# Kernel optimization log

Hardware: AMD Instinct MI355X
Metric: run time of the kernel (lower is better)

## Reference

```python
import jax, jax.numpy as jnp
import numpy as np

DIM = 512
HEADS = 8        # MultiHeadAttention default heads=8 (init 'heads' arg actually sets dim_head)
DIM_HEAD = 64    # from AttentionLayers heads=64 passed positionally as dim_head
HIDDEN = HEADS * DIM_HEAD  # 512
EPS = 1e-5


def setup_inputs() -> dict:
    key = jax.random.key(0)
    ks = jax.random.split(key, 8)
    s = 1.0 / np.sqrt(DIM)
    return {
        "x": jax.random.normal(ks[0], (4, 2048, DIM), dtype=jnp.float32),
        "ln_g": jnp.ones((DIM,), dtype=jnp.float32),
        "ln_b": jnp.zeros((DIM,), dtype=jnp.float32),
        "Wq": jax.random.normal(ks[1], (DIM, HIDDEN), dtype=jnp.float32) * s,
        "Wk": jax.random.normal(ks[2], (DIM, HIDDEN), dtype=jnp.float32) * s,
        "Wv": jax.random.normal(ks[3], (DIM, HIDDEN), dtype=jnp.float32) * s,
        "Wo": jax.random.normal(ks[4], (HIDDEN, DIM), dtype=jnp.float32) * s,
        "bo": jnp.zeros((DIM,), dtype=jnp.float32),
    }


def reference(x, ln_g, ln_b, Wq, Wk, Wv, Wo, bo):
    b, n, d = x.shape
    residual = x
    # pre-norm LayerNorm
    mu = jnp.mean(x, axis=-1, keepdims=True)
    var = jnp.mean((x - mu) ** 2, axis=-1, keepdims=True)
    xn = (x - mu) * jax.lax.rsqrt(var + EPS) * ln_g + ln_b
    # QKV projections (no bias), split into heads: [b, s, h, dh]
    q = (xn @ Wq).reshape(b, n, HEADS, DIM_HEAD)
    k = (xn @ Wk).reshape(b, n, HEADS, DIM_HEAD)
    v = (xn @ Wv).reshape(b, n, HEADS, DIM_HEAD)
    scale = HIDDEN ** (-0.5)  # note: scales by hidden_dim, not dim_head (faithful)
    scores = jnp.einsum('bihd,bjhd->bhij', q, k) * scale  # [b,h,i,j] full matrix
    attn = jax.nn.softmax(scores, axis=-1)
    out = jnp.einsum('bhij,bjhd->bihd', attn, v).reshape(b, n, HIDDEN)
    out = out @ Wo + bo
    # residual; the subsequent FFN layer's output is discarded in the source
    return out + residual
```

## Files before the change

kernel.cpp:

```cpp
#include <hip/hip_runtime.h>
#include <hip/hip_bf16.h>

#define DIM 512
#define SEQ 2048
#define BATCH 4
#define NHEADS 8
#define DH 64
#define NROWS (BATCH * SEQ)
#define LN_EPS 1e-5f

typedef __hip_bfloat16 bf16;
typedef __attribute__((ext_vector_type(8))) short short8;
typedef __attribute__((ext_vector_type(4))) float f32x4;

#define MFMA16(a, b, c) __builtin_amdgcn_mfma_f32_16x16x32_bf16((a), (b), (c), 0, 0, 0)

#if __has_builtin(__builtin_amdgcn_exp2f)
#define EXP2(x) __builtin_amdgcn_exp2f(x)
#else
#define EXP2(x) exp2f(x)
#endif

#if defined(__has_builtin)
#if __has_builtin(__builtin_amdgcn_global_load_lds)
#define HAS_GLDS 1
#endif
#endif

__device__ __forceinline__ void glds16(const bf16* g, bf16* l) {
#ifdef HAS_GLDS
  __builtin_amdgcn_global_load_lds((const __attribute__((address_space(1))) void*)g,
                                   (__attribute__((address_space(3))) void*)l, 16, 0, 0);
#else
  *reinterpret_cast<uint4*>(l) = *reinterpret_cast<const uint4*>(g);
#endif
}

__device__ __forceinline__ void store_bf16x4(bf16* p, float a, float b, float c, float d) {
  bf16 tmp[4] = {__float2bfloat16(a), __float2bfloat16(b), __float2bfloat16(c),
                 __float2bfloat16(d)};
  *reinterpret_cast<ushort4*>(p) = *reinterpret_cast<const ushort4*>(tmp);
}

#define Q_SCALE_LOG2E 0.06375872f

__global__ void ln_kernel(const float* __restrict__ x, const float* __restrict__ gamma,
                          const float* __restrict__ beta, bf16* __restrict__ xn) {
  const int row = blockIdx.x;
  const int t = threadIdx.x;
  const float2 v = reinterpret_cast<const float2*>(x + (size_t)row * DIM)[t];
  float s = v.x + v.y;
  float ss = v.x * v.x + v.y * v.y;
#pragma unroll
  for (int off = 32; off > 0; off >>= 1) {
    s += __shfl_down(s, off);
    ss += __shfl_down(ss, off);
  }
  __shared__ float red[8];
  __shared__ float stats[2];
  if ((t & 63) == 0) { red[(t >> 6) * 2] = s; red[(t >> 6) * 2 + 1] = ss; }
  __syncthreads();
  if (t == 0) {
    float S = red[0] + red[2] + red[4] + red[6];
    float SS = red[1] + red[3] + red[5] + red[7];
    float mu = S * (1.0f / DIM);
    float var = SS * (1.0f / DIM) - mu * mu;
    stats[0] = mu;
    stats[1] = rsqrtf(var + LN_EPS);
  }
  __syncthreads();
  const float mu = stats[0], rs = stats[1];
  const float2 gg = reinterpret_cast<const float2*>(gamma)[t];
  const float2 bb = reinterpret_cast<const float2*>(beta)[t];
  __hip_bfloat162 o;
  o.x = __float2bfloat16((v.x - mu) * rs * gg.x + bb.x);
  o.y = __float2bfloat16((v.y - mu) * rs * gg.y + bb.y);
  reinterpret_cast<__hip_bfloat162*>(xn + (size_t)row * DIM)[t] = o;
}

__global__ void wt_all_kernel(const float* __restrict__ Wq, const float* __restrict__ Wk,
                              const float* __restrict__ Wv, const float* __restrict__ Wo,
                              bf16* __restrict__ Wt) {
  const int z = blockIdx.z;
  const float* __restrict__ W = (z == 0) ? Wq : (z == 1) ? Wk : (z == 2) ? Wv : Wo;
  const float scale = (z == 0) ? Q_SCALE_LOG2E : 1.0f;
  bf16* __restrict__ dst = Wt + (size_t)z * DIM * DIM;
  __shared__ float tile[32][33];
  const int bx = blockIdx.x, by = blockIdx.y;
  const int tx = threadIdx.x & 31, ty = threadIdx.x >> 5;
#pragma unroll
  for (int i = 0; i < 32; i += 8)
    tile[ty + i][tx] = W[(size_t)(by * 32 + ty + i) * DIM + bx * 32 + tx];
  __syncthreads();
#pragma unroll
  for (int i = 0; i < 32; i += 8)
    dst[(size_t)(bx * 32 + ty + i) * DIM + by * 32 + tx] =
        __float2bfloat16(tile[tx][ty + i] * scale);
}

__launch_bounds__(256, 3)
__global__ void gemm_qkv_kernel(const bf16* __restrict__ A, const bf16* __restrict__ Bt,
                                bf16* __restrict__ qo, bf16* __restrict__ ko,
                                bf16* __restrict__ vo) {
  const int m0 = blockIdx.x * 128, n0g = blockIdx.y * 128;
  __shared__ __align__(16) bf16 sA[2][128 * 32];
  __shared__ __align__(16) bf16 sB[2][128 * 32];
  const int t = threadIdx.x, w = t >> 6, l = t & 63;
  const int r = l & 15, g = l >> 4;
  const int wm = w >> 1, wn = w & 1;
  const int crow = w * 32 + (l >> 2);
  const int ccol = (l & 3) * 8;
  const bf16* gA = A + (size_t)(m0 + crow) * DIM + ccol;
  const bf16* gB = Bt + (size_t)(n0g + crow) * DIM + ccol;
  const int loff = w * 1024 + l * 8;
  f32x4 acc[4][4] = {};
  glds16(gA, sA[0] + loff);
  glds16(gA + 16 * DIM, sA[0] + loff + 512);
  glds16(gB, sB[0] + loff);
  glds16(gB + 16 * DIM, sB[0] + loff + 512);
  const int NK = DIM / 32;
  for (int ks = 0; ks < NK; ks++) {
    const int cur = ks & 1;
    __syncthreads();
    if (ks + 1 < NK) {
      const int k0n = (ks + 1) * 32;
      glds16(gA + k0n, sA[1 - cur] + loff);
      glds16(gA + 16 * DIM + k0n, sA[1 - cur] + loff + 512);
      glds16(gB + k0n, sB[1 - cur] + loff);
      glds16(gB + 16 * DIM + k0n, sB[1 - cur] + loff + 512);
    }
    short8 af[4], bfv[4];
#pragma unroll
    for (int i = 0; i < 4; i++)
      af[i] = *reinterpret_cast<const short8*>(&sA[cur][(wm * 64 + i * 16 + r) * 32 + g * 8]);
#pragma unroll
    for (int j = 0; j < 4; j++)
      bfv[j] = *reinterpret_cast<const short8*>(&sB[cur][(wn * 64 + j * 16 + r) * 32 + g * 8]);
#pragma unroll
    for (int i = 0; i < 4; i++)
#pragma unroll
      for (int j = 0; j < 4; j++) acc[i][j] = MFMA16(af[i], bfv[j], acc[i][j]);
  }
  const int z = n0g >> 9;
  const int nc0 = (n0g & 511) + wn * 64;
  bf16* __restrict__ outp = (z == 0) ? qo : (z == 1) ? ko : vo;
#pragma unroll
  for (int i = 0; i < 4; i++)
#pragma unroll
    for (int j = 0; j < 4; j++)
#pragma unroll
      for (int reg = 0; reg < 4; reg++) {
        const int m = m0 + wm * 64 + i * 16 + g * 4 + reg;
        const int col = nc0 + j * 16 + r;
        outp[(size_t)m * DIM + col] = __float2bfloat16(acc[i][j][reg]);
      }
}

__global__ void vtrans_kernel(const bf16* __restrict__ v, bf16* __restrict__ vt) {
  __shared__ __align__(16) bf16 sT[64][72];
  const int s0 = blockIdx.x * 64, d0 = blockIdx.y * 64, b = blockIdx.z;
  const int t = threadIdx.x;
  const int row = t >> 2, col = (t & 3) * 8;
  const bf16* src = v + ((size_t)(b * SEQ) + s0 + row) * DIM + d0 + col;
  reinterpret_cast<uint4&>(sT[row][col]) = *reinterpret_cast<const uint4*>(src);
  reinterpret_cast<uint4&>(sT[row][col + 32]) = *reinterpret_cast<const uint4*>(src + 32);
  __syncthreads();
  const int drow = t >> 2, jcol = (t & 3) * 8;
  bf16 tmp[8], tmp2[8];
#pragma unroll
  for (int jj = 0; jj < 8; jj++) tmp[jj] = sT[jcol + jj][drow];
#pragma unroll
  for (int jj = 0; jj < 8; jj++) tmp2[jj] = sT[jcol + 32 + jj][drow];
  bf16* dst = vt + ((size_t)(b * DIM) + d0 + drow) * SEQ + s0 + jcol;
  *reinterpret_cast<uint4*>(dst) = *reinterpret_cast<const uint4*>(tmp);
  *reinterpret_cast<uint4*>(dst + 32) = *reinterpret_cast<const uint4*>(tmp2);
}

template <bool SPLIT>
__launch_bounds__(128, 3)
__global__ void attn_kernel(const bf16* __restrict__ q, const bf16* __restrict__ k,
                            const bf16* __restrict__ vt, bf16* __restrict__ ao,
                            bf16* __restrict__ opart, float* __restrict__ lpart) {
  const int it = blockIdx.x, bh = blockIdx.y, jh = blockIdx.z;
  const int b = bh >> 3, h = bh & 7;
  const int t = threadIdx.x, wv = t >> 6, l = t & 63;
  const int r = l & 15, g = l >> 4;
  __shared__ __align__(16) bf16 sK[64 * 64];
  __shared__ __align__(16) bf16 sV[64 * 64];
  __shared__ __align__(16) bf16 sPt[2][2][16][72];
  const int i0 = it * 64 + wv * 32;
  const bf16* qp = q + ((size_t)(b * SEQ) + i0 + r) * DIM + h * DH;
  short8 qf[2][2];
#pragma unroll
  for (int s = 0; s < 2; s++)
#pragma unroll
    for (int kc = 0; kc < 2; kc++)
      qf[s][kc] = *reinterpret_cast<const short8*>(qp + s * 16 * DIM + kc * 32 + g * 8);
  f32x4 oacc[2][4] = {};
  float lsum[2] = {0.f, 0.f};
  const int jbase = SPLIT ? jh * (SEQ / 2) : 0;
  const int srow8 = l >> 3;
  const int u = ((l & 7) - srow8) & 7;
  const bf16* kg = k + ((size_t)(b * SEQ) + jbase + wv * 32 + srow8) * DIM + h * DH + u * 8;
  const bf16* vg = vt + ((size_t)(b * DIM) + h * DH + wv * 32 + srow8) * SEQ + jbase + u * 8;
  const int loff = wv * 2048 + l * 8;
  const int e0 = 64 * r + 8 * ((g + r) & 7);
  const int e1 = 64 * r + 8 * ((4 + g + r) & 7);
  const int NJ = SPLIT ? (SEQ / 2) / 64 : SEQ / 64;
  for (int jt = 0; jt < NJ; jt++) {
    const int j0 = jt * 64;
#pragma unroll
    for (int cc = 0; cc < 4; cc++) {
      glds16(kg + (size_t)(j0 + cc * 8) * DIM, sK + loff + cc * 512);
      glds16(vg + (size_t)(cc * 8) * SEQ + j0, sV + loff + cc * 512);
    }
    __syncthreads();
    f32x4 st[2][4];
#pragma unroll
    for (int c = 0; c < 4; c++) {
      const short8 kf0 = *reinterpret_cast<const short8*>(sK + 1024 * c + e0);
      const short8 kf1 = *reinterpret_cast<const short8*>(sK + 1024 * c + e1);
#pragma unroll
      for (int s = 0; s < 2; s++) {
        f32x4 a = {0.f, 0.f, 0.f, 0.f};
        a = MFMA16(kf0, qf[s][0], a);
        a = MFMA16(kf1, qf[s][1], a);
        st[s][c] = a;
      }
    }
#pragma unroll
    for (int s = 0; s < 2; s++)
#pragma unroll
      for (int c = 0; c < 4; c++) {
        const float p0 = EXP2(st[s][c][0]);
        const float p1 = EXP2(st[s][c][1]);
        const float p2 = EXP2(st[s][c][2]);
        const float p3 = EXP2(st[s][c][3]);
        lsum[s] += (p0 + p1) + (p2 + p3);
        store_bf16x4(&sPt[wv][s][r][c * 16 + g * 4], p0, p1, p2, p3);
      }
#pragma unroll
    for (int kc2 = 0; kc2 < 2; kc2++) {
      short8 pf[2];
#pragma unroll
      for (int s = 0; s < 2; s++)
        pf[s] = *reinterpret_cast<const short8*>(&sPt[wv][s][r][kc2 * 32 + g * 8]);
      const int ev = (kc2 == 0) ? e0 : e1;
#pragma unroll
      for (int dt = 0; dt < 4; dt++) {
        const short8 vf = *reinterpret_cast<const short8*>(sV + 1024 * dt + ev);
#pragma unroll
        for (int s = 0; s < 2; s++) oacc[s][dt] = MFMA16(vf, pf[s], oacc[s][dt]);
      }
    }
    __syncthreads();
  }
#pragma unroll
  for (int s = 0; s < 2; s++) {
    lsum[s] += __shfl_xor(lsum[s], 16);
    lsum[s] += __shfl_xor(lsum[s], 32);
  }
  if (SPLIT) {
    const size_t obase = ((size_t)jh * 32 + bh) * SEQ;
#pragma unroll
    for (int s = 0; s < 2; s++) {
      const int i = i0 + s * 16 + r;
      if (l < 16) lpart[obase + i] = lsum[s];
#pragma unroll
      for (int dt = 0; dt < 4; dt++)
        store_bf16x4(opart + (obase + i) * 64 + dt * 16 + g * 4, oacc[s][dt][0],
                     oacc[s][dt][1], oacc[s][dt][2], oacc[s][dt][3]);
    }
  } else {
#pragma unroll
    for (int s = 0; s < 2; s++) {
      const float inv = 1.0f / lsum[s];
      const int i = i0 + s * 16 + r;
#pragma unroll
      for (int dt = 0; dt < 4; dt++)
        store_bf16x4(ao + ((size_t)(b * SEQ) + i) * DIM + h * DH + dt * 16 + g * 4,
                     oacc[s][dt][0] * inv, oacc[s][dt][1] * inv, oacc[s][dt][2] * inv,
                     oacc[s][dt][3] * inv);
    }
  }
}

__global__ void attn_combine_kernel(const bf16* __restrict__ opart,
                                    const float* __restrict__ lpart, bf16* __restrict__ ao) {
  const int bh = blockIdx.y, b = bh >> 3, h = bh & 7;
  const int t = threadIdx.x;
  const int i = blockIdx.x * 16 + (t >> 4);
  const int d = (t & 15) * 4;
  const size_t row0 = (size_t)bh * SEQ + i;
  const size_t row1 = ((size_t)32 + bh) * SEQ + i;
  const ushort4 a = *reinterpret_cast<const ushort4*>(opart + row0 * 64 + d);
  const ushort4 c = *reinterpret_cast<const ushort4*>(opart + row1 * 64 + d);
  const float inv = 1.0f / (lpart[row0] + lpart[row1]);
#define B2F(us) __uint_as_float(((unsigned)(us)) << 16)
  store_bf16x4(ao + ((size_t)(b * SEQ) + i) * DIM + h * DH + d,
               (B2F(a.x) + B2F(c.x)) * inv, (B2F(a.y) + B2F(c.y)) * inv,
               (B2F(a.z) + B2F(c.z)) * inv, (B2F(a.w) + B2F(c.w)) * inv);
#undef B2F
}

__launch_bounds__(256, 2)
__global__ void gemm_proj_kernel(const bf16* __restrict__ A, const bf16* __restrict__ Bt,
                                 const float* __restrict__ bo, const float* __restrict__ x,
                                 float* __restrict__ out) {
  const int m0 = blockIdx.x * 128, n0 = blockIdx.y * 64;
  __shared__ __align__(16) bf16 sA[2][128 * 32];
  __shared__ __align__(16) bf16 sB[2][64 * 32];
  const int t = threadIdx.x, w = t >> 6, l = t & 63;
  const int r = l & 15, g = l >> 4;
  const int wm = w >> 1, wn = w & 1;
  const int arow = t >> 2;
  const int ccol = (t & 3) * 8;
  const bf16* gA = A + (size_t)(m0 + arow) * DIM + ccol;
  const bf16* gB = Bt + (size_t)(n0 + arow) * DIM + ccol;
  const int loff = t * 8;
  f32x4 acc[4][2] = {};
  glds16(gA, sA[0] + loff);
  glds16(gA + 64 * DIM, sA[0] + loff + 2048);
  glds16(gB, sB[0] + loff);
  const int NK = DIM / 32;
  for (int ks = 0; ks < NK; ks++) {
    const int cur = ks & 1;
    __syncthreads();
    if (ks + 1 < NK) {
      const int k0n = (ks + 1) * 32;
      glds16(gA + k0n, sA[1 - cur] + loff);
      glds16(gA + 64 * DIM + k0n, sA[1 - cur] + loff + 2048);
      glds16(gB + k0n, sB[1 - cur] + loff);
    }
    short8 af[4], bfv[2];
#pragma unroll
    for (int i = 0; i < 4; i++)
      af[i] = *reinterpret_cast<const short8*>(&sA[cur][(wm * 64 + i * 16 + r) * 32 + g * 8]);
#pragma unroll
    for (int j = 0; j < 2; j++)
      bfv[j] = *reinterpret_cast<const short8*>(&sB[cur][(wn * 32 + j * 16 + r) * 32 + g * 8]);
#pragma unroll
    for (int i = 0; i < 4; i++)
#pragma unroll
      for (int j = 0; j < 2; j++) acc[i][j] = MFMA16(af[i], bfv[j], acc[i][j]);
  }
#pragma unroll
  for (int i = 0; i < 4; i++)
#pragma unroll
    for (int j = 0; j < 2; j++)
#pragma unroll
      for (int reg = 0; reg < 4; reg++) {
        const int m = m0 + wm * 64 + i * 16 + g * 4 + reg;
        const int col = n0 + wn * 32 + j * 16 + r;
        out[(size_t)m * DIM + col] = acc[i][j][reg] + bo[col] + x[(size_t)m * DIM + col];
      }
}

extern "C" void kernel_launch(void* const* d_in, const int* in_sizes, int n_in,
                              void* d_out, int out_size, void* d_ws, size_t ws_size,
                              hipStream_t stream) {
  (void)in_sizes; (void)n_in; (void)out_size;
  const float* x    = (const float*)d_in[0];
  const float* ln_g = (const float*)d_in[1];
  const float* ln_b = (const float*)d_in[2];
  const float* Wq   = (const float*)d_in[3];
  const float* Wk   = (const float*)d_in[4];
  const float* Wv   = (const float*)d_in[5];
  const float* Wo   = (const float*)d_in[6];
  const float* bo   = (const float*)d_in[7];
  float* out = (float*)d_out;
  char* ws = (char*)d_ws;
  bf16* xn  = (bf16*)(ws);
  bf16* vtb = (bf16*)(ws);
  bf16* wt  = (bf16*)(ws + (8u << 20));
  bf16* qb  = (bf16*)(ws + (10u << 20));
  bf16* kb  = (bf16*)(ws + (18u << 20));
  bf16* vb  = (bf16*)(ws + (26u << 20));
  bf16* aob = (bf16*)(ws + (34u << 20));
  bf16* opart = (bf16*)(ws + (42u << 20));
  float* lpart = (float*)(ws + (58u << 20));
  const bool split = ws_size >= ((58u << 20) + (1u << 19));

  ln_kernel<<<NROWS, 256, 0, stream>>>(x, ln_g, ln_b, xn);
  wt_all_kernel<<<dim3(16, 16, 4), 256, 0, stream>>>(Wq, Wk, Wv, Wo, wt);
  gemm_qkv_kernel<<<dim3(NROWS / 128, (3 * DIM) / 128), 256, 0, stream>>>(xn, wt, qb, kb, vb);
  vtrans_kernel<<<dim3(SEQ / 64, DIM / 64, BATCH), 256, 0, stream>>>(vb, vtb);
  if (split) {
    attn_kernel<true><<<dim3(SEQ / 64, BATCH * NHEADS, 2), 128, 0, stream>>>(
        qb, kb, vtb, aob, opart, lpart);
    attn_combine_kernel<<<dim3(SEQ / 16, BATCH * NHEADS), 256, 0, stream>>>(opart, lpart, aob);
  } else {
    attn_kernel<false><<<dim3(SEQ / 64, BATCH * NHEADS, 1), 128, 0, stream>>>(
        qb, kb, vtb, aob, opart, lpart);
  }
  gemm_proj_kernel<<<dim3(NROWS / 128, DIM / 64), 256, 0, stream>>>(aob, wt + 3 * DIM * DIM,
                                                                    bo, x, out);
}
```

Before: 186.4 us.

## Fuse V transpose into QKV GEMM epilogue and keep K/V tiles in registers

The QKV GEMM epilogue now writes V already transposed, going through a padded LDS tile, so the separate vtrans kernel and its extra global round trip are removed. The attention kernel no longer stages K and V through shared memory with barriers. Each lane loads its own MFMA fragments straight from global memory into registers and prefetches the next tile's fragments during compute. This removes LDS traffic and per-tile __syncthreads, but each wave now loads the K/V data itself, which raises redundant global/L2 traffic and register pressure.

Result: slower. 244.3 us (+31.0%).

```diff
diff --git a/kernel.cpp b/kernel.cpp
--- a/kernel.cpp
+++ b/kernel.cpp
@@ -101,10 +101,12 @@
 __launch_bounds__(256, 3)
 __global__ void gemm_qkv_kernel(const bf16* __restrict__ A, const bf16* __restrict__ Bt,
                                 bf16* __restrict__ qo, bf16* __restrict__ ko,
-                                bf16* __restrict__ vo) {
+                                bf16* __restrict__ vto) {
   const int m0 = blockIdx.x * 128, n0g = blockIdx.y * 128;
-  __shared__ __align__(16) bf16 sA[2][128 * 32];
-  __shared__ __align__(16) bf16 sB[2][128 * 32];
+  __shared__ __align__(16) char smem[128 * 136 * 2];
+  bf16* const sA = (bf16*)smem;
+  bf16* const sB = (bf16*)(smem + 16384);
+  bf16* const sT = (bf16*)smem;
   const int t = threadIdx.x, w = t >> 6, l = t & 63;
   const int r = l & 15, g = l >> 4;
   const int wm = w >> 1, wn = w & 1;
@@ -114,66 +116,68 @@
   const bf16* gB = Bt + (size_t)(n0g + crow) * DIM + ccol;
   const int loff = w * 1024 + l * 8;
   f32x4 acc[4][4] = {};
-  glds16(gA, sA[0] + loff);
-  glds16(gA + 16 * DIM, sA[0] + loff + 512);
-  glds16(gB, sB[0] + loff);
-  glds16(gB + 16 * DIM, sB[0] + loff + 512);
+  glds16(gA, sA + loff);
+  glds16(gA + 16 * DIM, sA + loff + 512);
+  glds16(gB, sB + loff);
+  glds16(gB + 16 * DIM, sB + loff + 512);
   const int NK = DIM / 32;
   for (int ks = 0; ks < NK; ks++) {
     const int cur = ks & 1;
     __syncthreads();
     if (ks + 1 < NK) {
       const int k0n = (ks + 1) * 32;
-      glds16(gA + k0n, sA[1 - cur] + loff);
-      glds16(gA + 16 * DIM + k0n, sA[1 - cur] + loff + 512);
-      glds16(gB + k0n, sB[1 - cur] + loff);
-      glds16(gB + 16 * DIM + k0n, sB[1 - cur] + loff + 512);
+      glds16(gA + k0n, sA + (1 - cur) * 4096 + loff);
+      glds16(gA + 16 * DIM + k0n, sA + (1 - cur) * 4096 + loff + 512);
+      glds16(gB + k0n, sB + (1 - cur) * 4096 + loff);
+      glds16(gB + 16 * DIM + k0n, sB + (1 - cur) * 4096 + loff + 512);
     }
     short8 af[4], bfv[4];
 #pragma unroll
     for (int i = 0; i < 4; i++)
-      af[i] = *reinterpret_cast<const short8*>(&sA[cur][(wm * 64 + i * 16 + r) * 32 + g * 8]);
+      af[i] = *reinterpret_cast<const short8*>(
+          &sA[cur * 4096 + (wm * 64 + i * 16 + r) * 32 + g * 8]);
 #pragma unroll
     for (int j = 0; j < 4; j++)
-      bfv[j] = *reinterpret_cast<const short8*>(&sB[cur][(wn * 64 + j * 16 + r) * 32 + g * 8]);
+      bfv[j] = *reinterpret_cast<const short8*>(
+          &sB[cur * 4096 + (wn * 64 + j * 16 + r) * 32 + g * 8]);
 #pragma unroll
     for (int i = 0; i < 4; i++)
 #pragma unroll
       for (int j = 0; j < 4; j++) acc[i][j] = MFMA16(af[i], bfv[j], acc[i][j]);
   }
   const int z = n0g >> 9;
-  const int nc0 = (n0g & 511) + wn * 64;
-  bf16* __restrict__ outp = (z == 0) ? qo : (z == 1) ? ko : vo;
-#pragma unroll
-  for (int i = 0; i < 4; i++)
-#pragma unroll
-    for (int j = 0; j < 4; j++)
-#pragma unroll
-      for (int reg = 0; reg < 4; reg++) {
-        const int m = m0 + wm * 64 + i * 16 + g * 4 + reg;
-        const int col = nc0 + j * 16 + r;
-        outp[(size_t)m * DIM + col] = __float2bfloat16(acc[i][j][reg]);
-      }
-}
-
-__global__ void vtrans_kernel(const bf16* __restrict__ v, bf16* __restrict__ vt) {
-  __shared__ __align__(16) bf16 sT[64][72];
-  const int s0 = blockIdx.x * 64, d0 = blockIdx.y * 64, b = blockIdx.z;
-  const int t = threadIdx.x;
-  const int row = t >> 2, col = (t & 3) * 8;
-  const bf16* src = v + ((size_t)(b * SEQ) + s0 + row) * DIM + d0 + col;
-  reinterpret_cast<uint4&>(sT[row][col]) = *reinterpret_cast<const uint4*>(src);
-  reinterpret_cast<uint4&>(sT[row][col + 32]) = *reinterpret_cast<const uint4*>(src + 32);
-  __syncthreads();
-  const int drow = t >> 2, jcol = (t & 3) * 8;
-  bf16 tmp[8], tmp2[8];
-#pragma unroll
-  for (int jj = 0; jj < 8; jj++) tmp[jj] = sT[jcol + jj][drow];
-#pragma unroll
-  for (int jj = 0; jj < 8; jj++) tmp2[jj] = sT[jcol + 32 + jj][drow];
-  bf16* dst = vt + ((size_t)(b * DIM) + d0 + drow) * SEQ + s0 + jcol;
-  *reinterpret_cast<uint4*>(dst) = *reinterpret_cast<const uint4*>(tmp);
-  *reinterpret_cast<uint4*>(dst + 32) = *reinterpret_cast<const uint4*>(tmp2);
+  const int b = m0 / SEQ;
+  if (z != 2) {
+    bf16* __restrict__ outp = (z == 0) ? qo : ko;
+    const int nc0 = (n0g & 511) + wn * 64;
+#pragma unroll
+    for (int i = 0; i < 4; i++)
+#pragma unroll
+      for (int j = 0; j < 4; j++)
+#pragma unroll
+        for (int reg = 0; reg < 4; reg++) {
+          const int m = m0 + wm * 64 + i * 16 + g * 4 + reg;
+          const int col = nc0 + j * 16 + r;
+          outp[(size_t)m * DIM + col] = __float2bfloat16(acc[i][j][reg]);
+        }
+  } else {
+    __syncthreads();
+#pragma unroll
+    for (int i = 0; i < 4; i++)
+#pragma unroll
+      for (int j = 0; j < 4; j++)
+        store_bf16x4(&sT[(wn * 64 + j * 16 + r) * 136 + wm * 64 + i * 16 + g * 4],
+                     acc[i][j][0], acc[i][j][1], acc[i][j][2], acc[i][j][3]);
+    __syncthreads();
+    const int dr = t >> 1;
+    const int mc = (t & 1) * 64;
+    const int dcol = (n0g & 511) + dr;
+    bf16* dst = vto + ((size_t)b * DIM + dcol) * SEQ + (m0 - b * SEQ) + mc;
+#pragma unroll
+    for (int uu = 0; uu < 8; uu++)
+      *reinterpret_cast<uint4*>(dst + uu * 8) =
+          *reinterpret_cast<const uint4*>(&sT[dr * 136 + mc + uu * 8]);
+  }
 }
 
 template <bool SPLIT>
@@ -185,9 +189,7 @@
   const int b = bh >> 3, h = bh & 7;
   const int t = threadIdx.x, wv = t >> 6, l = t & 63;
   const int r = l & 15, g = l >> 4;
-  __shared__ __align__(16) bf16 sK[64 * 64];
-  __shared__ __align__(16) bf16 sV[64 * 64];
-  __shared__ __align__(16) bf16 sPt[2][2][16][72];
+  __shared__ __align__(16) bf16 sPt[2][2][16][76];
   const int i0 = it * 64 + wv * 32;
   const bf16* qp = q + ((size_t)(b * SEQ) + i0 + r) * DIM + h * DH;
   short8 qf[2][2];
@@ -199,27 +201,27 @@
   f32x4 oacc[2][4] = {};
   float lsum[2] = {0.f, 0.f};
   const int jbase = SPLIT ? jh * (SEQ / 2) : 0;
-  const int srow8 = l >> 3;
-  const int u = ((l & 7) - srow8) & 7;
-  const bf16* kg = k + ((size_t)(b * SEQ) + jbase + wv * 32 + srow8) * DIM + h * DH + u * 8;
-  const bf16* vg = vt + ((size_t)(b * DIM) + h * DH + wv * 32 + srow8) * SEQ + jbase + u * 8;
-  const int loff = wv * 2048 + l * 8;
-  const int e0 = 64 * r + 8 * ((g + r) & 7);
-  const int e1 = 64 * r + 8 * ((4 + g + r) & 7);
+  const bf16* kl = k + ((size_t)(b * SEQ) + jbase + r) * DIM + h * DH + g * 8;
+  const bf16* vl = vt + ((size_t)(b * DIM) + h * DH + r) * SEQ + jbase + g * 8;
+  uint4 kr[8], vr[8];
+#pragma unroll
+  for (int c = 0; c < 4; c++)
+#pragma unroll
+    for (int hf = 0; hf < 2; hf++)
+      kr[c * 2 + hf] = *reinterpret_cast<const uint4*>(kl + (size_t)(c * 16) * DIM + hf * 32);
+#pragma unroll
+  for (int dt = 0; dt < 4; dt++)
+#pragma unroll
+    for (int kc2 = 0; kc2 < 2; kc2++)
+      vr[dt * 2 + kc2] =
+          *reinterpret_cast<const uint4*>(vl + (size_t)(dt * 16) * SEQ + kc2 * 32);
   const int NJ = SPLIT ? (SEQ / 2) / 64 : SEQ / 64;
   for (int jt = 0; jt < NJ; jt++) {
-    const int j0 = jt * 64;
-#pragma unroll
-    for (int cc = 0; cc < 4; cc++) {
-      glds16(kg + (size_t)(j0 + cc * 8) * DIM, sK + loff + cc * 512);
-      glds16(vg + (size_t)(cc * 8) * SEQ + j0, sV + loff + cc * 512);
-    }
-    __syncthreads();
     f32x4 st[2][4];
 #pragma unroll
     for (int c = 0; c < 4; c++) {
-      const short8 kf0 = *reinterpret_cast<const short8*>(sK + 1024 * c + e0);
-      const short8 kf1 = *reinterpret_cast<const short8*>(sK + 1024 * c + e1);
+      const short8 kf0 = *reinterpret_cast<const short8*>(&kr[c * 2 + 0]);
+      const short8 kf1 = *reinterpret_cast<const short8*>(&kr[c * 2 + 1]);
 #pragma unroll
       for (int s = 0; s < 2; s++) {
         f32x4 a = {0.f, 0.f, 0.f, 0.f};
@@ -227,6 +229,15 @@
         a = MFMA16(kf1, qf[s][1], a);
         st[s][c] = a;
       }
+    }
+    if (jt + 1 < NJ) {
+      const int jo = (jt + 1) * 64;
+#pragma unroll
+      for (int c = 0; c < 4; c++)
+#pragma unroll
+        for (int hf = 0; hf < 2; hf++)
+          kr[c * 2 + hf] =
+              *reinterpret_cast<const uint4*>(kl + (size_t)(jo + c * 16) * DIM + hf * 32);
     }
 #pragma unroll
     for (int s = 0; s < 2; s++)
@@ -245,15 +256,22 @@
 #pragma unroll
       for (int s = 0; s < 2; s++)
         pf[s] = *reinterpret_cast<const short8*>(&sPt[wv][s][r][kc2 * 32 + g * 8]);
-      const int ev = (kc2 == 0) ? e0 : e1;
 #pragma unroll
       for (int dt = 0; dt < 4; dt++) {
-        const short8 vf = *reinterpret_cast<const short8*>(sV + 1024 * dt + ev);
+        const short8 vf = *reinterpret_cast<const short8*>(&vr[dt * 2 + kc2]);
 #pragma unroll
         for (int s = 0; s < 2; s++) oacc[s][dt] = MFMA16(vf, pf[s], oacc[s][dt]);
       }
     }
-    __syncthreads();
+    if (jt + 1 < NJ) {
+      const int jo = (jt + 1) * 64;
+#pragma unroll
+      for (int dt = 0; dt < 4; dt++)
+#pragma unroll
+        for (int kc2 = 0; kc2 < 2; kc2++)
+          vr[dt * 2 + kc2] =
+              *reinterpret_cast<const uint4*>(vl + (size_t)(dt * 16) * SEQ + jo + kc2 * 32);
+    }
   }
 #pragma unroll
   for (int s = 0; s < 2; s++) {
@@ -371,11 +389,10 @@
   float* out = (float*)d_out;
   char* ws = (char*)d_ws;
   bf16* xn  = (bf16*)(ws);
-  bf16* vtb = (bf16*)(ws);
   bf16* wt  = (bf16*)(ws + (8u << 20));
   bf16* qb  = (bf16*)(ws + (10u << 20));
   bf16* kb  = (bf16*)(ws + (18u << 20));
-  bf16* vb  = (bf16*)(ws + (26u << 20));
+  bf16* vtb = (bf16*)(ws + (26u << 20));
   bf16* aob = (bf16*)(ws + (34u << 20));
   bf16* opart = (bf16*)(ws + (42u << 20));
   float* lpart = (float*)(ws + (58u << 20));
@@ -383,8 +400,7 @@
 
   ln_kernel<<<NROWS, 256, 0, stream>>>(x, ln_g, ln_b, xn);
   wt_all_kernel<<<dim3(16, 16, 4), 256, 0, stream>>>(Wq, Wk, Wv, Wo, wt);
-  gemm_qkv_kernel<<<dim3(NROWS / 128, (3 * DIM) / 128), 256, 0, stream>>>(xn, wt, qb, kb, vb);
-  vtrans_kernel<<<dim3(SEQ / 64, DIM / 64, BATCH), 256, 0, stream>>>(vb, vtb);
+  gemm_qkv_kernel<<<dim3(NROWS / 128, (3 * DIM) / 128), 256, 0, stream>>>(xn, wt, qb, kb, vtb);
   if (split) {
     attn_kernel<true><<<dim3(SEQ / 64, BATCH * NHEADS, 2), 128, 0, stream>>>(
         qb, kb, vtb, aob, opart, lpart);
```
